# Performance work log

Hardware: AMD Instinct MI355X
Metric: run time of the kernel (lower is better)

## Reference

```python
import jax, jax.numpy as jnp
import numpy as np

# Fixed hierarchical grouping of the 15 regions into 5 groups of 3 (from split_regions)
SPLIT_IDX = np.array([[0, 1, 8], [2, 4, 6], [3, 5, 7], [9, 11, 13], [10, 12, 14]])
BN_EPS = 1e-5


def _bn_relu(x, g, b):
    # BatchNorm over (batch, spatial) dims in training-stats mode, then ReLU
    mu = jnp.mean(x, axis=(0, 2, 3), keepdims=True)
    var = jnp.var(x, axis=(0, 2, 3), keepdims=True)
    xn = (x - mu) * jax.lax.rsqrt(var + BN_EPS)
    return jax.nn.relu(xn * g[None, :, None, None] + b[None, :, None, None])


def _local_agg(x, params):
    # x: [B, Cin, G, K]; pointwise conv (1x1) -> BN -> ReLU per layer, then max over K
    for W, g, b in params:
        x = jnp.einsum('oi,bigk->bogk', W, x)
        x = _bn_relu(x, g, b)
    return jnp.max(x, axis=-1)  # [B, Cout, G]


def setup_inputs() -> dict:
    key = jax.random.key(0)
    ks = jax.random.split(key, 8)
    B, G, K = 32, 15, 2048
    inp = {"local_regions": jax.random.normal(ks[0], (B, G, K, 3), jnp.float32)}
    chans = [(3, 64, 64), (67, 128, 128), (131, 256, 256)]
    ki = 1
    for li, (c0, c1, c2) in enumerate(chans):
        for wi, (co, ci) in enumerate([(c1, c0), (c2, c1)]):
            inp[f"la{li}_w{wi}"] = jax.random.normal(ks[ki], (co, ci), jnp.float32) * (1.0 / np.sqrt(ci))
            inp[f"la{li}_g{wi}"] = jnp.ones((co,), jnp.float32)
            inp[f"la{li}_b{wi}"] = jnp.zeros((co,), jnp.float32)
            ki += 1
    return inp


def reference(local_regions,
              la0_w0, la0_g0, la0_b0, la0_w1, la0_g1, la0_b1,
              la1_w0, la1_g0, la1_b0, la1_w1, la1_g1, la1_b1,
              la2_w0, la2_g0, la2_b0, la2_w1, la2_g1, la2_b1):
    la0 = [(la0_w0, la0_g0, la0_b0), (la0_w1, la0_g1, la0_b1)]
    la1 = [(la1_w0, la1_g0, la1_b0), (la1_w1, la1_g1, la1_b1)]
    la2 = [(la2_w0, la2_g0, la2_b0), (la2_w1, la2_g1, la2_b1)]
    idx = jnp.asarray(SPLIT_IDX)

    x = jnp.transpose(local_regions, (0, 3, 1, 2))  # [B, 3, 15, K]
    centroids_1 = jnp.mean(x, axis=-1)              # [B, 3, 15]
    relative_1 = x - centroids_1[..., None]
    lf1 = _local_agg(relative_1, la0)               # [B, 64, 15]
    local_features = jnp.concatenate([centroids_1, lf1], axis=1)  # [B, 67, 15]

    # level 2: regroup 15 regions into [5, 3]
    lf1_s = jnp.transpose(lf1, (0, 2, 1))[:, idx, :]         # [B, 5, 3, 64]
    lr2 = jnp.transpose(centroids_1, (0, 2, 1))[:, idx, :]   # [B, 5, 3, 3]
    c2 = jnp.mean(lr2, axis=2)                               # [B, 5, 3]
    rel2 = lr2 - c2[:, :, None, :]
    feats2 = jnp.concatenate([rel2, lf1_s], axis=-1)         # [B, 5, 3, 67]
    feats2 = jnp.transpose(feats2, (0, 3, 1, 2))             # [B, 67, 5, 3]
    lf2 = _local_agg(feats2, la1)                            # [B, 128, 5]

    # level 3: global
    c3 = jnp.mean(c2, axis=1)                                # [B, 3]
    rel3 = c2 - c3[:, None, :]                               # [B, 5, 3]
    lf2 = jnp.concatenate([jnp.transpose(rel3, (0, 2, 1)), lf2], axis=1)  # [B, 131, 5]
    lf2 = lf2[:, :, None, :]                                 # [B, 131, 1, 5]
    gf = _local_agg(lf2, la2)                                # [B, 256, 1]
    return gf.squeeze(2), local_features
```

## Files before the change

### kernel.cpp

```cpp
#include <hip/hip_runtime.h>
#include <math.h>

#define GG 15
#define KK 2048
#define NB 480
#define N1F 983040.0f
#define EPS 1e-5f
#define PZN ((int)0xAAAAAAAA)

typedef _Float16 half8 __attribute__((ext_vector_type(8)));
typedef float f32x4 __attribute__((ext_vector_type(4)));

#define CENT  0
#define GSREL 1920
#define GBN1  2160
#define SELO  6256
#define FBN1  36976
#define H2A   37104
#define H2B   98544
#define H3A   159984
#define H3B   200944
#define GS2A  241904
#define GS2B  242416
#define GS3A  242928
#define GS3B  243952
#define CFLG  244976
#define ARRB  247856

#define SMEMF 7936

__device__ const int SIDX[15] = {0,1,8, 2,4,6, 3,5,7, 9,11,13, 10,12,14};

__device__ __forceinline__ float wave_sum(float v){
    for (int off = 32; off; off >>= 1) v += __shfl_down(v, off, 64);
    return v;
}
__device__ __forceinline__ float aloadf(const float* p){
    return __hip_atomic_load(p, __ATOMIC_RELAXED, __HIP_MEMORY_SCOPE_AGENT);
}
__device__ __forceinline__ int aloadi(const int* p){
    return __hip_atomic_load(p, __ATOMIC_RELAXED, __HIP_MEMORY_SCOPE_AGENT);
}
template<int SLP, class Fold, class Pref>
__device__ __forceinline__ void sbar(int* wsi, int idx, int gi, int bid,
                                     int* sflag, Fold fold, Pref pref){
    __syncthreads();
    if (threadIdx.x == 0)
        atomicExch(&wsi[ARRB + (idx*480 + bid)*16], 1);
    if (bid == 0) {
        int guard = 0, done = 0;
        do {
            int ok = 1;
            for (int s = threadIdx.x; s < 480; s += 256)
                ok &= (aloadi(&wsi[ARRB + (idx*480 + s)*16]) == 1) ? 1 : 0;
            ok = __all(ok) ? 1 : 0;
            if ((threadIdx.x & 63) == 0) sflag[2 + (threadIdx.x >> 6)] = ok;
            __syncthreads();
            done = sflag[2] & sflag[3] & sflag[4] & sflag[5];
            __syncthreads();
            if (!done) __builtin_amdgcn_s_sleep(SLP);
        } while (!done && ++guard < 4000000);
        fold();
        __syncthreads();
        if (threadIdx.x < 30)
            atomicExch(&wsi[CFLG + (idx*30 + threadIdx.x)*16], 1);
        pref();
    } else {
        pref();
    }
    if (threadIdx.x == 0) {
        int g = 0;
        while (aloadi(&wsi[CFLG + (idx*30 + gi)*16]) != 1 && ++g < 8000000)
            __builtin_amdgcn_s_sleep(SLP);
    }
    __syncthreads();
    asm volatile("" ::: "memory");
}
struct NoF { __device__ void operator()() const {} };

__global__ void __launch_bounds__(256, 2) mega(
        const float* __restrict__ x,
        const float* __restrict__ w00, const float* __restrict__ g00, const float* __restrict__ b00,
        const float* __restrict__ w01, const float* __restrict__ g01, const float* __restrict__ b01,
        const float* __restrict__ w10, const float* __restrict__ g10, const float* __restrict__ b10,
        const float* __restrict__ w11, const float* __restrict__ g11, const float* __restrict__ b11,
        const float* __restrict__ w20, const float* __restrict__ g20, const float* __restrict__ b20,
        const float* __restrict__ w21, const float* __restrict__ g21, const float* __restrict__ b21,
        float* __restrict__ ws, float* __restrict__ out) {
    __shared__ __align__(16) float smemf[SMEMF];
    float* xls  = smemf;
    float* redM = smemf + 6144; float* redN = smemf + 6400;
    float* redS = smemf + 6656; float* redQ = smemf + 6912;
    float* bcast= smemf + 7168;
    int*   sflag= (int*)(smemf + 7916);
    float* s1ls  = smemf;
    float* t1ls  = smemf + 64;
    float* centb = smemf + 128;
    float* c2b   = smemf + 176;
    float* c3b   = smemf + 192;
    float* f2b   = smemf + 256;
    float* wstg  = smemf + 256;
    float* vls   = smemf + 1424;
    float* f3b   = smemf + 3360;
    float* u3b   = smemf + 4020;
    float* c2s   = smemf + 5312;
    float* c2t   = smemf + 5440;
    float* s4ls  = smemf + 5568;
    float* t4ls  = smemf + 5824;
    float* w10st = smemf + 6144;
    float* hst   = smemf + 6912;
    int* wsi = (int*)ws;

    int bid = blockIdx.x, tid = threadIdx.x;
    int b_ = bid / GG, g_ = bid % GG;
    int wv = tid >> 6, lane = tid & 63, l15 = lane & 15, quad = lane >> 4;
    int gi = bid >> 4;
    int sgrp = b_ >> 4;
    int cg = (g_ + 14) % 15;
    int base2 = cg*9,  nr2 = (cg == 14) ? 2 : 9;
    int base3 = cg*18, nr3 = (cg == 14) ? 4 : 18;
    int stq = (nr3 < 12) ? nr3 : 12;

    {
        const float4* xp4 = (const float4*)(x + (size_t)bid * KK * 3);
        float4* xls4 = (float4*)xls;
        #pragma unroll
        for (int i = 0; i < 6; i++) xls4[i*256 + tid] = xp4[i*256 + tid];
        __syncthreads();
        float m[9] = {0,0,0,0,0,0,0,0,0};
        float a[24];
        const float* bp = &xls[tid*24];
        #pragma unroll
        for (int i = 0; i < 6; i++)
            *reinterpret_cast<float4*>(&a[i*4]) = *reinterpret_cast<const float4*>(&bp[i*4]);
        #pragma unroll
        for (int p = 0; p < 8; p++) {
            float ax=a[p*3], ay=a[p*3+1], az=a[p*3+2];
            m[0]+=ax; m[1]+=ay; m[2]+=az;
            m[3]=fmaf(ax,ax,m[3]); m[4]=fmaf(ay,ay,m[4]); m[5]=fmaf(az,az,m[5]);
            m[6]=fmaf(ax,ay,m[6]); m[7]=fmaf(ax,az,m[7]); m[8]=fmaf(ay,az,m[8]);
        }
        #pragma unroll
        for (int q = 0; q < 9; q++) {
            float v = wave_sum(m[q]);
            if (lane == 0) redM[q*4 + wv] = v;
        }
        __syncthreads();
        if (tid == 0) {
            float t[9];
            #pragma unroll
            for (int q = 0; q < 9; q++) t[q] = redM[q*4]+redM[q*4+1]+redM[q*4+2]+redM[q*4+3];
            float c0 = t[0]/KK, c1 = t[1]/KK, c2 = t[2]/KK;
            bcast[0]=c0; bcast[1]=c1; bcast[2]=c2;
            out[8192 + b_*(67*GG) + 0*GG + g_] = c0;
            out[8192 + b_*(67*GG) + 1*GG + g_] = c1;
            out[8192 + b_*(67*GG) + 2*GG + g_] = c2;
            atomicExch(&ws[CENT + bid*4 + 0], c0);
            atomicExch(&ws[CENT + bid*4 + 1], c1);
            atomicExch(&ws[CENT + bid*4 + 2], c2);
            redM[40] = t[3] - KK*c0*c0;  redM[41] = t[4] - KK*c1*c1;
            redM[42] = t[5] - KK*c2*c2;  redM[43] = t[6] - KK*c0*c1;
            redM[44] = t[7] - KK*c0*c2;  redM[45] = t[8] - KK*c1*c2;
        }
        __syncthreads();
    }
    if (tid < 6) atomicAdd(&ws[GSREL + gi*8 + tid], redM[40 + tid]);

    half8 afA[4], afB[4];
    #pragma unroll
    for (int t = 0; t < 4; t++)
        #pragma unroll
        for (int j = 0; j < 8; j++) {
            afA[t][j] = (_Float16)w01[(t*16 + l15)*64 + quad*8 + j];
            afB[t][j] = (_Float16)w01[(t*16 + l15)*64 + 32 + quad*8 + j];
        }

    sbar<1>(wsi, 0, gi, bid, sflag, NoF{}, NoF{});

    if (tid < 6) {
        float acc = 0.f;
        #pragma unroll
        for (int s = 0; s < 30; s++) acc += aloadf(&ws[GSREL + s*8 + tid]);
        bcast[3+tid] = acc / N1F;
    }
    __syncthreads();
    float c0 = bcast[0], c1 = bcast[1], c2v = bcast[2];
    float S00=bcast[3], S11=bcast[4], S22=bcast[5], S01=bcast[6], S02=bcast[7], S12=bcast[8];

    float wa0[8], wa1[8], wa2[8], ba[8], wb0[8], wb1[8], wb2[8], bb[8];
    #pragma unroll
    for (int j = 0; j < 8; j++) {
        int cA = quad*8 + j;
        float u0=w00[cA*3+0], u1=w00[cA*3+1], u2=w00[cA*3+2];
        float var = u0*u0*S00 + u1*u1*S11 + u2*u2*S22
                  + 2.f*(u0*u1*S01 + u0*u2*S02 + u1*u2*S12);
        float a1 = g00[cA]*rsqrtf(var + EPS);
        wa0[j]=a1*u0; wa1[j]=a1*u1; wa2[j]=a1*u2; ba[j]=b00[cA];
        int cB = cA + 32;
        float v0=w00[cB*3+0], v1=w00[cB*3+1], v2=w00[cB*3+2];
        float varB = v0*v0*S00 + v1*v1*S11 + v2*v2*S22
                   + 2.f*(v0*v1*S01 + v0*v2*S02 + v1*v2*S12);
        float a1B = g00[cB]*rsqrtf(varB + EPS);
        wb0[j]=a1B*v0; wb1[j]=a1B*v1; wb2[j]=a1B*v2; bb[j]=b00[cB];
    }
    float mx[16], mn[16], sm[16], sq[16];
    #pragma unroll
    for (int s = 0; s < 16; s++) { mx[s]=-1e30f; mn[s]=1e30f; sm[s]=0.f; sq[s]=0.f; }

    for (int it = 0; it < 32; it++) {
        int k = it*64 + wv*16 + l15;
        float r0 = xls[k*3+0]-c0, r1 = xls[k*3+1]-c1, r2 = xls[k*3+2]-c2v;
        half8 bf0, bf1;
        #pragma unroll
        for (int j = 0; j < 8; j++) {
            float pA = fmaf(wa0[j],r0, fmaf(wa1[j],r1, fmaf(wa2[j],r2, ba[j])));
            bf0[j] = (_Float16)fmaxf(pA, 0.f);
            float pB = fmaf(wb0[j],r0, fmaf(wb1[j],r1, fmaf(wb2[j],r2, bb[j])));
            bf1[j] = (_Float16)fmaxf(pB, 0.f);
        }
        #pragma unroll
        for (int t = 0; t < 4; t++) {
            f32x4 acc = {0.f,0.f,0.f,0.f};
            acc = __builtin_amdgcn_mfma_f32_16x16x32_f16(afA[t], bf0, acc, 0, 0, 0);
            acc = __builtin_amdgcn_mfma_f32_16x16x32_f16(afB[t], bf1, acc, 0, 0, 0);
            #pragma unroll
            for (int r = 0; r < 4; r++) {
                float h = acc[r];
                int s = t*4 + r;
                mx[s]=fmaxf(mx[s],h); mn[s]=fminf(mn[s],h);
                sm[s]+=h;             sq[s]=fmaf(h,h,sq[s]);
            }
        }
    }
    #pragma unroll
    for (int m = 1; m < 16; m <<= 1) {
        #pragma unroll
        for (int s = 0; s < 16; s++) {
            mx[s] = fmaxf(mx[s], __shfl_xor(mx[s], m, 64));
            mn[s] = fminf(mn[s], __shfl_xor(mn[s], m, 64));
            sm[s] += __shfl_xor(sm[s], m, 64);
            sq[s] += __shfl_xor(sq[s], m, 64);
        }
    }
    __syncthreads();
    if (l15 == 0) {
        #pragma unroll
        for (int t = 0; t < 4; t++)
            #pragma unroll
            for (int r = 0; r < 4; r++) {
                int o = t*16 + quad*4 + r;
                redM[wv*64+o]=mx[t*4+r]; redN[wv*64+o]=mn[t*4+r];
                redS[wv*64+o]=sm[t*4+r]; redQ[wv*64+o]=sq[t*4+r];
            }
    }
    __syncthreads();
    float Mreg = -1e30f, Nreg = 1e30f;
    if (tid < 64) {
        float S=0.f, Q=0.f;
        #pragma unroll
        for (int w = 0; w < 4; w++) {
            Mreg = fmaxf(Mreg, redM[w*64+tid]); Nreg = fminf(Nreg, redN[w*64+tid]);
            S += redS[w*64+tid];               Q += redQ[w*64+tid];
        }
        atomicAdd(&ws[GBN1 + b_*128 + tid], S);
        atomicAdd(&ws[GBN1 + b_*128 + 64 + tid], Q);
        float sel = (g01[tid] >= 0.f) ? Mreg : Nreg;
        atomicExch(&ws[SELO + bid*64 + tid], sel);
    }

    sbar<1>(wsi, 1, gi, bid, sflag, [&]{
        if (tid < 128) {
            float acc = 0.f;
            #pragma unroll
            for (int i = 0; i < 32; i++) acc += aloadf(&ws[GBN1 + i*128 + tid]);
            atomicExch(&ws[FBN1 + tid], acc);
        }
    }, [&]{
        for (int u = tid; u < nr2*67; u += 256) w10st[u] = w10[base2*67 + u];
    });

    if (tid < 64) {
        float S = aloadf(&ws[FBN1 + tid]);
        float Q = aloadf(&ws[FBN1 + 64 + tid]);
        float mean = S / N1F;
        float var  = Q / N1F - mean*mean;
        float s1 = g01[tid]*rsqrtf(var + EPS);
        float t1 = b01[tid] - mean*s1;
        float val = fmaxf(fmaf(s1, (s1 >= 0.f) ? Mreg : Nreg, t1), 0.f);
        out[8192 + b_*(67*GG) + (3+tid)*GG + g_] = val;
        s1ls[tid] = s1; t1ls[tid] = t1;
    }

    if (tid < 45) centb[tid] = aloadf(&ws[CENT + (b_*GG + tid/3)*4 + tid%3]);
    __syncthreads();
    if (tid < 15) {
        int s = tid/3, i = tid%3;
        c2b[tid] = (centb[SIDX[s*3+0]*3+i] + centb[SIDX[s*3+1]*3+i]
                  + centb[SIDX[s*3+2]*3+i]) * (1.f/3.f);
    }
    __syncthreads();
    if (tid < 3)
        c3b[tid] = (c2b[tid]+c2b[3+tid]+c2b[6+tid]+c2b[9+tid]+c2b[12+tid]) * 0.2f;
    if (tid < 45) {
        int p = tid/3, i = tid%3;
        f2b[p*69 + i] = centb[SIDX[p]*3+i] - c2b[(p/3)*3 + i];
    }
    for (int u = tid; u < 960; u += 256) {
        int p = u >> 6, ch = u & 63, src = b_*GG + SIDX[p];
        float sel = aloadf(&ws[SELO + src*64 + ch]);
        f2b[p*69 + 3 + ch] = fmaxf(fmaf(s1ls[ch], sel, t1ls[ch]), 0.f);
    }
    __syncthreads();
    if (tid < nr2*15) {
        int rl = tid/15, p = tid%15, r = base2 + rl;
        const float* wr = &w10st[rl*67];
        const float* fp = &f2b[p*69];
        float h = 0.f;
        #pragma unroll 4
        for (int c = 0; c < 67; c++) h = fmaf(wr[c], fp[c], h);
        atomicExch(&ws[H2A + (b_*GG + p)*128 + r], h);
        hst[rl*15 + p] = h;
    }
    __syncthreads();
    if (tid < nr2) {
        int r = base2 + tid;
        float S = 0.f, Q = 0.f;
        #pragma unroll
        for (int p = 0; p < 15; p++) { float v = hst[tid*15+p]; S += v; Q = fmaf(v,v,Q); }
        atomicAdd(&ws[GS2A + sgrp*256 + r], S);
        atomicAdd(&ws[GS2A + sgrp*256 + 128 + r], Q);
    }
    sbar<1>(wsi, 2, gi, bid, sflag, NoF{}, [&]{
        for (int u = tid; u < nr2*128; u += 256)
            wstg[(u>>7)*129 + (u&127)] = w11[base2*128 + u];
    });

    if (tid < 128) {
        float S = aloadf(&ws[GS2A + tid])       + aloadf(&ws[GS2A + 256 + tid]);
        float Q = aloadf(&ws[GS2A + 128 + tid]) + aloadf(&ws[GS2A + 256 + 128 + tid]);
        float mean = S / 480.f, var = Q / 480.f - mean*mean;
        float s2 = g10[tid]*rsqrtf(var + EPS);
        c2s[tid] = s2; c2t[tid] = b10[tid] - mean*s2;
    }
    __syncthreads();
    for (int u = tid; u < 1920; u += 256) {
        int p = u >> 7, ch = u & 127;
        float hv = aloadf(&ws[H2A + (b_*GG + p)*128 + ch]);
        vls[p*129 + ch] = fmaxf(fmaf(c2s[ch], hv, c2t[ch]), 0.f);
    }
    __syncthreads();
    if (tid < nr2*15) {
        int rl = tid/15, p = tid%15, r = base2 + rl;
        const float* wr = &wstg[rl*129];
        const float* vp = &vls[p*129];
        float h = 0.f;
        #pragma unroll 4
        for (int c = 0; c < 128; c++) h = fmaf(wr[c], vp[c], h);
        atomicExch(&ws[H2B + (b_*GG + p)*128 + r], h);
        hst[rl*15 + p] = h;
    }
    __syncthreads();
    if (tid < nr2) {
        int r = base2 + tid;
        float S = 0.f, Q = 0.f;
        #pragma unroll
        for (int p = 0; p < 15; p++) { float v = hst[tid*15+p]; S += v; Q = fmaf(v,v,Q); }
        atomicAdd(&ws[GS2B + sgrp*256 + r], S);
        atomicAdd(&ws[GS2B + sgrp*256 + 128 + r], Q);
    }
    sbar<1>(wsi, 3, gi, bid, sflag, NoF{}, [&]{
        for (int u = tid; u < nr3*131; u += 256) wstg[u] = w20[base3*131 + u];
    });

    if (tid < 128) {
        float S = aloadf(&ws[GS2B + tid])       + aloadf(&ws[GS2B + 256 + tid]);
        float Q = aloadf(&ws[GS2B + 128 + tid]) + aloadf(&ws[GS2B + 256 + 128 + tid]);
        float mean = S / 480.f, var = Q / 480.f - mean*mean;
        float s3 = g11[tid]*rsqrtf(var + EPS);
        c2s[tid] = s3; c2t[tid] = b11[tid] - mean*s3;
    }
    __syncthreads();
    for (int u = tid; u < 640; u += 256) {
        int s = u >> 7, ch = u & 127;
        float sv = c2s[ch], tv = c2t[ch], m = -1e30f;
        #pragma unroll
        for (int j = 0; j < 3; j++) {
            float hv = aloadf(&ws[H2B + (b_*GG + 3*s + j)*128 + ch]);
            m = fmaxf(m, fmaxf(fmaf(sv, hv, tv), 0.f));
        }
        f3b[s*132 + 3 + ch] = m;
    }
    if (tid < 15) {
        int s = tid/3, i = tid%3;
        f3b[s*132 + i] = c2b[tid] - c3b[i];
    }
    __syncthreads();
    if (tid < nr3*5) {
        int rl = tid/5, s = tid%5, r = base3 + rl;
        const float* wr = &wstg[rl*131];
        const float* fp = &f3b[s*132];
        float h = 0.f;
        #pragma unroll 4
        for (int c = 0; c < 131; c++) h = fmaf(wr[c], fp[c], h);
        atomicExch(&ws[H3A + (b_*5 + s)*256 + r], h);
        hst[rl*5 + s] = h;
    }
    __syncthreads();
    if (tid < nr3) {
        int r = base3 + tid;
        float S = 0.f, Q = 0.f;
        #pragma unroll
        for (int s = 0; s < 5; s++) { float v = hst[tid*5+s]; S += v; Q = fmaf(v,v,Q); }
        atomicAdd(&ws[GS3A + sgrp*512 + r], S);
        atomicAdd(&ws[GS3A + sgrp*512 + 256 + r], Q);
    }
    sbar<1>(wsi, 4, gi, bid, sflag, NoF{}, [&]{
        for (int u = tid; u < stq*256; u += 256)
            wstg[(u>>8)*257 + (u&255)] = w21[base3*256 + u];
    });

    {
        float S = aloadf(&ws[GS3A + tid])       + aloadf(&ws[GS3A + 512 + tid]);
        float Q = aloadf(&ws[GS3A + 256 + tid]) + aloadf(&ws[GS3A + 512 + 256 + tid]);
        float mean = S / 160.f, var = Q / 160.f - mean*mean;
        float s4 = g20[tid]*rsqrtf(var + EPS);
        s4ls[tid] = s4; t4ls[tid] = b20[tid] - mean*s4;
    }
    __syncthreads();
    for (int u = tid; u < 1280; u += 256) {
        int s = u >> 8, ch = u & 255;
        float hv = aloadf(&ws[H3A + (b_*5 + s)*256 + ch]);
        u3b[s*257 + ch] = fmaxf(fmaf(s4ls[ch], hv, t4ls[ch]), 0.f);
    }
    __syncthreads();
    if (tid < nr3*5) {
        int rl = tid/5, s = tid%5, r = base3 + rl;
        const float* up = &u3b[s*257];
        float h = 0.f;
        if (rl < 12) {
            const float* wr = &wstg[rl*257];
            #pragma unroll 4
            for (int c = 0; c < 256; c++) h = fmaf(wr[c], up[c], h);
        } else {
            const float* wr = w21 + (size_t)r*256;
            #pragma unroll 4
            for (int c = 0; c < 256; c++) h = fmaf(wr[c], up[c], h);
        }
        atomicExch(&ws[H3B + (b_*5 + s)*256 + r], h);
        hst[rl*5 + s] = h;
    }
    __syncthreads();
    if (tid < nr3) {
        int r = base3 + tid;
        float S = 0.f, Q = 0.f;
        #pragma unroll
        for (int s = 0; s < 5; s++) { float v = hst[tid*5+s]; S += v; Q = fmaf(v,v,Q); }
        atomicAdd(&ws[GS3B + sgrp*512 + r], S);
        atomicAdd(&ws[GS3B + sgrp*512 + 256 + r], Q);
    }
    sbar<1>(wsi, 5, gi, bid, sflag, NoF{}, NoF{});

    if (g_ == 0) {
        float S = aloadf(&ws[GS3B + tid])       + aloadf(&ws[GS3B + 512 + tid]);
        float Q = aloadf(&ws[GS3B + 256 + tid]) + aloadf(&ws[GS3B + 512 + 256 + tid]);
        float mean = S / 160.f, var = Q / 160.f - mean*mean;
        float s5 = g21[tid]*rsqrtf(var + EPS);
        float t5 = b21[tid] - mean*s5;
        float m = -1e30f;
        #pragma unroll
        for (int s = 0; s < 5; s++) {
            float hv = aloadf(&ws[H3B + (b_*5 + s)*256 + tid]);
            m = fmaxf(m, fmaxf(fmaf(s5, hv, t5), 0.f));
        }
        out[b_*256 + tid] = m;
    }
}

extern "C" void kernel_launch(void* const* d_in, const int* in_sizes, int n_in,
                              void* d_out, int out_size, void* d_ws, size_t ws_size,
                              hipStream_t stream) {
    (void)in_sizes; (void)n_in; (void)out_size; (void)ws_size;
    const float* x   = (const float*)d_in[0];
    const float* w00 = (const float*)d_in[1];
    const float* g00 = (const float*)d_in[2];
    const float* b00 = (const float*)d_in[3];
    const float* w01 = (const float*)d_in[4];
    const float* g01 = (const float*)d_in[5];
    const float* b01 = (const float*)d_in[6];
    const float* w10 = (const float*)d_in[7];
    const float* g10 = (const float*)d_in[8];
    const float* b10 = (const float*)d_in[9];
    const float* w11 = (const float*)d_in[10];
    const float* g11 = (const float*)d_in[11];
    const float* b11 = (const float*)d_in[12];
    const float* w20 = (const float*)d_in[13];
    const float* g20 = (const float*)d_in[14];
    const float* b20 = (const float*)d_in[15];
    const float* w21 = (const float*)d_in[16];
    const float* g21 = (const float*)d_in[17];
    const float* b21 = (const float*)d_in[18];
    float* out = (float*)d_out;
    float* ws  = (float*)d_ws;

    mega<<<NB, 256, 0, stream>>>(x, w00,g00,b00, w01,g01,b01, w10,g10,b10,
                                 w11,g11,b11, w20,g20,b20, w21,g21,b21, ws, out);
}
```

Measured before the change: 172.2 us.

## Use hierarchical two-level arrival tree for grid barrier

Replaces the flat grid barrier, where block 0 polled all 480 per-block arrival flags, with a two-level tree. The first block of each 16-block group waits for its group's flags and then sets a group-done flag, and block 0 polls only the 30 group flags before folding. This shortens block 0's polling loop and spreads the flag reads across groups. In exchange it adds more spinning blocks and one extra flag hop of latency per barrier, and it depends on the GDON workspace region being large enough and reset between runs.

New measurement: 172.9 us. No clear change (+0.4%).

```diff
diff --git a/kernel.cpp b/kernel.cpp
--- a/kernel.cpp
+++ b/kernel.cpp
@@ -26,6 +26,7 @@
 #define GS3B  243952
 #define CFLG  244976
 #define ARRB  247856
+#define GDON  293936
 
 #define SMEMF 7936
 
@@ -47,19 +48,30 @@
     __syncthreads();
     if (threadIdx.x == 0)
         atomicExch(&wsi[ARRB + (idx*480 + bid)*16], 1);
+    if ((bid & 15) == 0 && threadIdx.x < 64) {
+        int g = 0;
+        for (;;) {
+            int ok = (threadIdx.x < 16)
+                ? (aloadi(&wsi[ARRB + (idx*480 + gi*16 + threadIdx.x)*16]) == 1)
+                : 1;
+            if (__all(ok) || ++g >= 8000000) break;
+            __builtin_amdgcn_s_sleep(SLP);
+        }
+        if (threadIdx.x == 0)
+            atomicExch(&wsi[GDON + (idx*30 + gi)*16], 1);
+    }
     if (bid == 0) {
-        int guard = 0, done = 0;
-        do {
-            int ok = 1;
-            for (int s = threadIdx.x; s < 480; s += 256)
-                ok &= (aloadi(&wsi[ARRB + (idx*480 + s)*16]) == 1) ? 1 : 0;
-            ok = __all(ok) ? 1 : 0;
-            if ((threadIdx.x & 63) == 0) sflag[2 + (threadIdx.x >> 6)] = ok;
-            __syncthreads();
-            done = sflag[2] & sflag[3] & sflag[4] & sflag[5];
-            __syncthreads();
-            if (!done) __builtin_amdgcn_s_sleep(SLP);
-        } while (!done && ++guard < 4000000);
+        if (threadIdx.x < 64) {
+            int g = 0;
+            for (;;) {
+                int ok = (threadIdx.x < 30)
+                    ? (aloadi(&wsi[GDON + (idx*30 + threadIdx.x)*16]) == 1)
+                    : 1;
+                if (__all(ok) || ++g >= 8000000) break;
+                __builtin_amdgcn_s_sleep(SLP);
+            }
+        }
+        __syncthreads();
         fold();
         __syncthreads();
         if (threadIdx.x < 30)
```
